# Optimization experiments

Hardware: AMD Instinct MI355X
Metric: run time of the kernel (lower is better)

Reference implementation:

```python
import jax, jax.numpy as jnp
import numpy as np

B, K, D, H = 16384, 3, 1024, 16
DH = D // H  # head_dim = 64


def setup_inputs() -> dict:
    key = jax.random.key(0)
    ks = jax.random.split(key, 12)
    s = 1.0 / np.sqrt(D)
    inp = {
        "tokens": jax.random.normal(ks[0], (B, K, D), dtype=jnp.float32),
        "ctx": jax.random.normal(ks[1], (B, 1, D), dtype=jnp.float32),
        "Wq": jax.random.uniform(ks[2], (D, D), jnp.float32, -s, s),
        "bq": jnp.zeros((D,), jnp.float32),
        "Wk": jax.random.uniform(ks[3], (D, D), jnp.float32, -s, s),
        "bk": jnp.zeros((D,), jnp.float32),
        "Wv": jax.random.uniform(ks[4], (D, D), jnp.float32, -s, s),
        "bv": jnp.zeros((D,), jnp.float32),
        "Wc": jax.random.uniform(ks[5], (D, D), jnp.float32, -s, s),
        "bc": jnp.zeros((D,), jnp.float32),
        "Wo": jax.random.uniform(ks[6], (D, D), jnp.float32, -s, s),
        "bo": jnp.zeros((D,), jnp.float32),
    }
    return inp


def _split_heads(x):
    # (B, L, D) -> (B, H, L, DH)
    Bq, L, _ = x.shape
    return x.reshape(Bq, L, H, DH).transpose(0, 2, 1, 3)


def reference(tokens, ctx, Wq, bq, Wk, bk, Wv, bv, Wc, bc, Wo, bo):
    q = _split_heads(tokens @ Wq.T + bq)          # (B,H,K,DH)
    k = _split_heads(tokens @ Wk.T + bk)          # (B,H,K,DH)
    v = _split_heads(tokens @ Wv.T + bv)          # (B,H,K,DH)
    c = _split_heads(ctx @ Wc.T + bc)             # (B,H,1,DH)
    k_ctx = k * c                                  # context-modulated keys
    v_ctx = v * c                                  # context-modulated values
    scores = jnp.einsum("bhqd,bhkd->bhqk", q, k_ctx) / jnp.sqrt(jnp.float32(DH))
    probs = jax.nn.softmax(scores, axis=-1)       # dropout p=0.0 -> identity
    out = jnp.einsum("bhqk,bhkd->bhqd", probs, v_ctx)
    out = out.transpose(0, 2, 1, 3).reshape(tokens.shape[0], K, D)  # merge heads
    return out @ Wo.T + bo
```

## Files before the change

### kernel.cpp

```cpp
#include <hip/hip_runtime.h>
#include <hip/hip_bf16.h>

#define BB 16384
#define KK 3
#define DD 1024
#define HH 16

typedef __attribute__((ext_vector_type(8))) short bf16x8;
typedef __attribute__((ext_vector_type(4))) float f32x4;
typedef unsigned int u32;

__device__ __forceinline__ void load_lds16(const void* g, void* l) {
  __builtin_amdgcn_global_load_lds(
      (const __attribute__((address_space(1))) u32*)g,
      (__attribute__((address_space(3))) u32*)l,
      16, 0, 0);
}

__device__ __forceinline__ unsigned short f2bf(float f) {
  __hip_bfloat16 h = __float2bfloat16(f);
  unsigned short u;
  __builtin_memcpy(&u, &h, 2);
  return u;
}

__device__ __forceinline__ float bf2f(unsigned short u) {
  union { float f; u32 i; } cv;
  cv.i = ((u32)u) << 16;
  return cv.f;
}

__global__ void cast_f32_bf16(const float* __restrict__ in,
                              unsigned short* __restrict__ out, int n4) {
  int stride = gridDim.x * blockDim.x;
  for (int i = blockIdx.x * blockDim.x + threadIdx.x; i < n4; i += stride) {
    float4 v = ((const float4*)in)[i];
    ushort4 o;
    o.x = f2bf(v.x);
    o.y = f2bf(v.y);
    o.z = f2bf(v.z);
    o.w = f2bf(v.w);
    ((ushort4*)out)[i] = o;
  }
}

template <bool OUT_F32>
__global__ __launch_bounds__(512, 2)
void gemm256(const __hip_bfloat16* __restrict__ A,
             const __hip_bfloat16* __restrict__ Bt,
             const float* __restrict__ bias,
             void* __restrict__ Cout,
             int M, int N, int K) {
  __shared__ __align__(128) char lds[131072];

  const int nTn = N >> 8;
  const int nwg = (M >> 8) * nTn;
  int bid = blockIdx.x;
  bid = (bid & 7) * (nwg >> 3) + (bid >> 3);
  const int tm = bid / nTn;
  const int tn = bid % nTn;

  const int tid = threadIdx.x;
  const int l = tid & 63;
  const int w = tid >> 6;
  const int wm = w >> 2;
  const int wn = w & 3;
  const int l15 = l & 15;
  const int g = l >> 4;
  const int l7 = l15 & 7;

  const int cs0 = ((g ^ l7) << 4);
  const int cs1 = (((4 | g) ^ l7) << 4);
  const int aRowB = ((wm << 7) + l15) << 7;
  const int bColB = 32768 + (((wn << 6) + l15) << 7);

  const size_t strideK = (size_t)K * 2;
  const char* Ab = (const char*)A + (size_t)tm * 256 * strideK;
  const char* Bb = (const char*)Bt + (size_t)tn * 256 * strideK;
  const size_t sOff = (size_t)(tid >> 3) * strideK +
                      (size_t)(((tid & 7) ^ ((tid >> 3) & 7)) << 4);
  const int sldst = tid << 4;

  char* const sl0 = lds;
  char* const sl1 = lds + 65536;

  f32x4 acc[8][4] = {};
  bf16x8 aF[16], bF[8];
  const int njt = K >> 7;

#define STG_A(T, H)                                                        \
  {                                                                        \
    char* d = lds + (((T) & 1) << 16) + ((H) << 14) + sldst;               \
    const char* s = Ab + ((size_t)(T) << 7) +                              \
                    ((size_t)((H) << 7)) * strideK + sOff;                 \
    load_lds16(s, d);                                                      \
    load_lds16(s + 64 * strideK, d + 8192);                                \
  }
#define STG_B(T, H)                                                        \
  {                                                                        \
    char* d = lds + (((T) & 1) << 16) + 32768 + ((H) << 14) + sldst;       \
    const char* s = Bb + ((size_t)(T) << 7) +                              \
                    ((size_t)((H) << 7)) * strideK + sOff;                 \
    load_lds16(s, d);                                                      \
    load_lds16(s + 64 * strideK, d + 8192);                                \
  }
#define RD_A2(SB, m)                                                       \
  aF[2 * (m)] = *(const bf16x8*)((SB) + aRowB + ((m) << 11) + cs0);        \
  aF[2 * (m) + 1] = *(const bf16x8*)((SB) + aRowB + ((m) << 11) + cs1);
#define RD_B2(SB, n)                                                       \
  bF[2 * (n)] = *(const bf16x8*)((SB) + bColB + ((n) << 11) + cs0);        \
  bF[2 * (n) + 1] = *(const bf16x8*)((SB) + bColB + ((n) << 11) + cs1);
#define MFMA_Q(MH, NH)                                                     \
  __builtin_amdgcn_s_setprio(1);                                           \
  _Pragma("unroll") for (int mm = 0; mm < 4; ++mm)                         \
      _Pragma("unroll") for (int nn = 0; nn < 2; ++nn)                     \
          _Pragma("unroll") for (int kh = 0; kh < 2; ++kh)                 \
              acc[(MH)*4 + mm][(NH)*2 + nn] =                              \
                  __builtin_amdgcn_mfma_f32_16x16x32_bf16(                 \
                      aF[2 * ((MH)*4 + mm) + kh],                          \
                      bF[2 * ((NH)*2 + nn) + kh],                          \
                      acc[(MH)*4 + mm][(NH)*2 + nn], 0, 0, 0);             \
  __builtin_amdgcn_s_setprio(0);
#define BAR  __builtin_amdgcn_s_barrier(); asm volatile("" ::: "memory");
#define LGKM0 asm volatile("s_waitcnt lgkmcnt(0)" ::: "memory");

  STG_A(0, 0); STG_A(0, 1); STG_B(0, 0); STG_B(0, 1);
  STG_A(1, 0); STG_A(1, 1);
  asm volatile("s_waitcnt vmcnt(4)" ::: "memory");
  BAR

  for (int j = 0; j < njt; ++j) {
    const int t1 = 2 * j + 1, t2 = 2 * j + 2, t3 = 2 * j + 3;
    const bool full = (j < njt - 1);

    RD_B2(sl0, 0) RD_B2(sl0, 1)
    RD_A2(sl0, 0) RD_A2(sl0, 1) RD_A2(sl0, 2) RD_A2(sl0, 3)
    STG_B(t1, 0)
    BAR LGKM0 MFMA_Q(0, 0) BAR
    RD_A2(sl0, 4) RD_A2(sl0, 5) RD_A2(sl0, 6) RD_A2(sl0, 7)
    STG_B(t1, 1)
    BAR LGKM0 MFMA_Q(1, 0) BAR
    RD_B2(sl0, 2) RD_B2(sl0, 3)
    if (full) STG_A(t2, 0)
    BAR LGKM0 MFMA_Q(0, 1) BAR
    if (full) STG_A(t2, 1)
    if (full) { asm volatile("s_waitcnt vmcnt(4)" ::: "memory"); }
    else      { asm volatile("s_waitcnt vmcnt(0)" ::: "memory"); }
    BAR MFMA_Q(1, 1) BAR

    RD_B2(sl1, 0) RD_B2(sl1, 1)
    RD_A2(sl1, 0) RD_A2(sl1, 1) RD_A2(sl1, 2) RD_A2(sl1, 3)
    if (full) STG_B(t2, 0)
    BAR LGKM0 MFMA_Q(0, 0) BAR
    RD_A2(sl1, 4) RD_A2(sl1, 5) RD_A2(sl1, 6) RD_A2(sl1, 7)
    if (full) STG_B(t2, 1)
    BAR LGKM0 MFMA_Q(1, 0) BAR
    RD_B2(sl1, 2) RD_B2(sl1, 3)
    if (full) STG_A(t3, 0)
    BAR LGKM0 MFMA_Q(0, 1) BAR
    if (full) STG_A(t3, 1)
    if (full) { asm volatile("s_waitcnt vmcnt(4)" ::: "memory"); }
    else      { asm volatile("s_waitcnt vmcnt(0)" ::: "memory"); }
    BAR MFMA_Q(1, 1) BAR
  }
#undef STG_A
#undef STG_B
#undef RD_A2
#undef RD_B2
#undef MFMA_Q
#undef BAR
#undef LGKM0

  const int cbase = tn * 256 + (wn << 6) + l15;
  float b4[4];
#pragma unroll
  for (int n = 0; n < 4; ++n) b4[n] = bias[cbase + (n << 4)];
  const size_t rbase = (size_t)tm * 256 + (wm << 7) + ((l >> 4) << 2);
#pragma unroll
  for (int m = 0; m < 8; ++m) {
#pragma unroll
    for (int j = 0; j < 4; ++j) {
      const size_t row = rbase + (m << 4) + j;
#pragma unroll
      for (int n = 0; n < 4; ++n) {
        const int col = cbase + (n << 4);
        float v = acc[m][n][j] + b4[n];
        if (OUT_F32)
          ((float*)Cout)[row * N + col] = v;
        else
          ((unsigned short*)Cout)[row * N + col] = f2bf(v);
      }
    }
  }
}

__global__ __launch_bounds__(256)
void attn_kernel(const unsigned short* __restrict__ QKV,
                 const unsigned short* __restrict__ Cp,
                 unsigned short* __restrict__ Out) {
  const int t = threadIdx.x;
  const int grp = (blockIdx.x << 4) + (t >> 4);
  const int x = t & 15;
  const int b = grp >> 4;
  const int h = grp & 15;

  const size_t col = (size_t)h * 64 + (x << 2);
  const size_t qbase = (size_t)b * 3 * 3072 + col;

  ushort4 cu = *(const ushort4*)&Cp[(size_t)b * 1024 + col];
  float c[4] = {bf2f(cu.x), bf2f(cu.y), bf2f(cu.z), bf2f(cu.w)};

  float q[3][4], kc[3][4], vc[3][4];
#pragma unroll
  for (int i = 0; i < 3; ++i) {
    ushort4 qu = *(const ushort4*)&QKV[qbase + (size_t)i * 3072];
    ushort4 ku = *(const ushort4*)&QKV[qbase + (size_t)i * 3072 + 1024];
    ushort4 vu = *(const ushort4*)&QKV[qbase + (size_t)i * 3072 + 2048];
    q[i][0] = bf2f(qu.x); q[i][1] = bf2f(qu.y); q[i][2] = bf2f(qu.z); q[i][3] = bf2f(qu.w);
    kc[i][0] = bf2f(ku.x) * c[0]; kc[i][1] = bf2f(ku.y) * c[1];
    kc[i][2] = bf2f(ku.z) * c[2]; kc[i][3] = bf2f(ku.w) * c[3];
    vc[i][0] = bf2f(vu.x) * c[0]; vc[i][1] = bf2f(vu.y) * c[1];
    vc[i][2] = bf2f(vu.z) * c[2]; vc[i][3] = bf2f(vu.w) * c[3];
  }

  float s[9];
#pragma unroll
  for (int i = 0; i < 3; ++i)
#pragma unroll
    for (int j = 0; j < 3; ++j)
      s[i * 3 + j] = q[i][0] * kc[j][0] + q[i][1] * kc[j][1] +
                     q[i][2] * kc[j][2] + q[i][3] * kc[j][3];

#pragma unroll
  for (int off = 8; off > 0; off >>= 1)
#pragma unroll
    for (int e = 0; e < 9; ++e)
      s[e] += __shfl_xor(s[e], off, 64);

  const float scale = 0.125f;
#pragma unroll
  for (int i = 0; i < 3; ++i) {
    float s0 = s[i * 3 + 0] * scale;
    float s1 = s[i * 3 + 1] * scale;
    float s2 = s[i * 3 + 2] * scale;
    float m = fmaxf(fmaxf(s0, s1), s2);
    float p0 = expf(s0 - m), p1 = expf(s1 - m), p2 = expf(s2 - m);
    float inv = 1.0f / (p0 + p1 + p2);
    ushort4 o;
    o.x = f2bf((p0 * vc[0][0] + p1 * vc[1][0] + p2 * vc[2][0]) * inv);
    o.y = f2bf((p0 * vc[0][1] + p1 * vc[1][1] + p2 * vc[2][1]) * inv);
    o.z = f2bf((p0 * vc[0][2] + p1 * vc[1][2] + p2 * vc[2][2]) * inv);
    o.w = f2bf((p0 * vc[0][3] + p1 * vc[1][3] + p2 * vc[2][3]) * inv);
    *(ushort4*)&Out[(size_t)(b * 3 + i) * 1024 + col] = o;
  }
}

extern "C" void kernel_launch(void* const* d_in, const int* in_sizes, int n_in,
                              void* d_out, int out_size, void* d_ws, size_t ws_size,
                              hipStream_t stream) {
  const float* tokens = (const float*)d_in[0];
  const float* ctx    = (const float*)d_in[1];
  const float* Wq     = (const float*)d_in[2];
  const float* bq     = (const float*)d_in[3];
  const float* Wk     = (const float*)d_in[4];
  const float* bk     = (const float*)d_in[5];
  const float* Wv     = (const float*)d_in[6];
  const float* bv     = (const float*)d_in[7];
  const float* Wc     = (const float*)d_in[8];
  const float* bc     = (const float*)d_in[9];
  const float* Wo     = (const float*)d_in[10];
  const float* bo     = (const float*)d_in[11];

  const int M  = BB * KK;
  const int Mc = BB;
  const int D  = DD;

  char* p = (char*)d_ws;
  auto carve = [&](size_t bytes) {
    char* r = p;
    p += (bytes + 255) & ~(size_t)255;
    return r;
  };
  unsigned short* Xb   = (unsigned short*)carve((size_t)M * D * 2);
  unsigned short* Cin  = (unsigned short*)carve((size_t)Mc * D * 2);
  unsigned short* Wqkv = (unsigned short*)carve((size_t)3 * D * D * 2);
  unsigned short* Wcb  = (unsigned short*)carve((size_t)D * D * 2);
  unsigned short* Wob  = (unsigned short*)carve((size_t)D * D * 2);
  float*          bqkv = (float*)carve((size_t)3 * D * 4);
  unsigned short* QKV  = (unsigned short*)carve((size_t)M * 3 * D * 2);
  unsigned short* Cpr  = (unsigned short*)carve((size_t)Mc * D * 2);

  hipLaunchKernelGGL(cast_f32_bf16, dim3(4096), dim3(256), 0, stream, tokens, Xb, M * D / 4);
  hipLaunchKernelGGL(cast_f32_bf16, dim3(2048), dim3(256), 0, stream, ctx, Cin, Mc * D / 4);
  hipLaunchKernelGGL(cast_f32_bf16, dim3(512), dim3(256), 0, stream, Wq, Wqkv, D * D / 4);
  hipLaunchKernelGGL(cast_f32_bf16, dim3(512), dim3(256), 0, stream, Wk, Wqkv + D * D, D * D / 4);
  hipLaunchKernelGGL(cast_f32_bf16, dim3(512), dim3(256), 0, stream, Wv, Wqkv + 2 * D * D, D * D / 4);
  hipLaunchKernelGGL(cast_f32_bf16, dim3(512), dim3(256), 0, stream, Wc, Wcb, D * D / 4);
  hipLaunchKernelGGL(cast_f32_bf16, dim3(512), dim3(256), 0, stream, Wo, Wob, D * D / 4);
  hipMemcpyAsync(bqkv, bq, D * 4, hipMemcpyDeviceToDevice, stream);
  hipMemcpyAsync(bqkv + D, bk, D * 4, hipMemcpyDeviceToDevice, stream);
  hipMemcpyAsync(bqkv + 2 * D, bv, D * 4, hipMemcpyDeviceToDevice, stream);

  hipLaunchKernelGGL((gemm256<false>), dim3((M / 256) * (3 * D / 256)), dim3(512), 0, stream,
                     (const __hip_bfloat16*)Xb, (const __hip_bfloat16*)Wqkv, bqkv,
                     (void*)QKV, M, 3 * D, D);
  hipLaunchKernelGGL((gemm256<false>), dim3((Mc / 256) * (D / 256)), dim3(512), 0, stream,
                     (const __hip_bfloat16*)Cin, (const __hip_bfloat16*)Wcb, bc,
                     (void*)Cpr, Mc, D, D);
  hipLaunchKernelGGL(attn_kernel, dim3(BB * HH / 16), dim3(256), 0, stream, QKV, Cpr, Xb);
  hipLaunchKernelGGL((gemm256<true>), dim3((M / 256) * (D / 256)), dim3(512), 0, stream,
                     (const __hip_bfloat16*)Xb, (const __hip_bfloat16*)Wob, bo,
                     d_out, M, D, D);
}
```

Measured before the change: 628.1 us.

## Fuse activation fp32-to-bf16 cast into GEMM A-loading and batch weight casts

Removes the separate cast kernels for tokens and ctx. A new GEMM kernel instead reads fp32 A directly into registers, converts it to bf16 and writes it into swizzled LDS, while B still arrives through direct global-to-LDS loads. The five weight casts are merged into one launch. This saves a full write and re-read of the bf16 activation copies. In exchange, the GEMM reads twice as many A bytes and uses a simpler double-buffered pipeline that may hide latency less well than the original gemm256.

```diff
diff --git a/kernel.cpp b/kernel.cpp
--- a/kernel.cpp
+++ b/kernel.cpp
@@ -30,17 +30,153 @@
   return cv.f;
 }
 
-__global__ void cast_f32_bf16(const float* __restrict__ in,
-                              unsigned short* __restrict__ out, int n4) {
-  int stride = gridDim.x * blockDim.x;
-  for (int i = blockIdx.x * blockDim.x + threadIdx.x; i < n4; i += stride) {
-    float4 v = ((const float4*)in)[i];
+__global__ __launch_bounds__(256)
+void cast_weights5(const float* __restrict__ Wq, const float* __restrict__ Wk,
+                   const float* __restrict__ Wv, const float* __restrict__ Wc,
+                   const float* __restrict__ Wo,
+                   unsigned short* __restrict__ Wqkv,
+                   unsigned short* __restrict__ Wcb,
+                   unsigned short* __restrict__ Wob) {
+  const int mat = blockIdx.x >> 8;
+  const int inner = blockIdx.x & 255;
+  const float* src = mat == 0 ? Wq : mat == 1 ? Wk : mat == 2 ? Wv
+                   : mat == 3 ? Wc : Wo;
+  unsigned short* dst = mat <= 2 ? Wqkv + (size_t)mat * DD * DD
+                      : mat == 3 ? Wcb : Wob;
+  const int base = inner * 1024 + threadIdx.x;
+#pragma unroll
+  for (int k = 0; k < 4; ++k) {
+    const int i = base + k * 256;
+    float4 v = ((const float4*)src)[i];
     ushort4 o;
-    o.x = f2bf(v.x);
-    o.y = f2bf(v.y);
-    o.z = f2bf(v.z);
-    o.w = f2bf(v.w);
-    ((ushort4*)out)[i] = o;
+    o.x = f2bf(v.x); o.y = f2bf(v.y); o.z = f2bf(v.z); o.w = f2bf(v.w);
+    ((ushort4*)dst)[i] = o;
+  }
+}
+
+__global__ __launch_bounds__(512, 2)
+void gemm_f32a(const float* __restrict__ A,
+               const __hip_bfloat16* __restrict__ Bt,
+               const float* __restrict__ bias,
+               unsigned short* __restrict__ Cout,
+               int M, int N, int K) {
+  __shared__ __align__(128) char lds[65536];
+
+  const int nTn = N >> 8;
+  const int nwg = (M >> 8) * nTn;
+  int bid = blockIdx.x;
+  bid = (bid & 7) * (nwg >> 3) + (bid >> 3);
+  const int tm = bid / nTn;
+  const int tn = bid % nTn;
+
+  const int tid = threadIdx.x;
+  const int l = tid & 63;
+  const int w = tid >> 6;
+  const int wm = w >> 2;
+  const int wn = w & 3;
+  const int l15 = l & 15;
+  const int g = l >> 4;
+  const int l7 = l15 & 7;
+
+  const int aBase = (l15 << 7) + (((wm << 2) + g) ^ l7) * 16;
+  const int bBase = 16384 + ((((wn & 1) << 6) + l15) << 7) +
+                    ((((wn >> 1) << 2) + g) ^ l7) * 16;
+
+  const int qa = tid & 7;
+  const int r1 = ((qa >> 2) << 7) + (tid >> 3);
+  const float* As = A + ((size_t)(tm * 256 + r1)) * K + ((qa & 3) << 3);
+  const int da = ((r1 & 127) << 7) + ((qa ^ (r1 & 7)) << 4);
+
+  const size_t strideB = (size_t)K * 2;
+  const char* Bb = (const char*)Bt + (size_t)tn * 256 * strideB;
+  const int qb = (tid & 7) ^ ((tid >> 3) & 7);
+  const size_t gb0 = (size_t)((qb >> 2) * 128 + (tid >> 3)) * strideB +
+                     (size_t)((qb & 3) << 4);
+  const size_t gb1 = gb0 + (size_t)64 * strideB;
+  const int sld = tid << 4;
+
+  f32x4 acc[8][4] = {};
+  float a0[8], a1[8];
+  const int nkt = K >> 5;
+
+#define LOAD_A(T)                                                         \
+  {                                                                       \
+    const float* s = As + ((T) << 5);                                     \
+    *(float4*)&a0[0] = *(const float4*)(s);                               \
+    *(float4*)&a0[4] = *(const float4*)(s + 4);                           \
+    *(float4*)&a1[0] = *(const float4*)(s + (size_t)64 * K);              \
+    *(float4*)&a1[4] = *(const float4*)(s + (size_t)64 * K + 4);          \
+  }
+#define LOAD_B(T)                                                         \
+  {                                                                       \
+    char* sb = lds + (((T) & 1) << 15);                                   \
+    const char* gbp = Bb + ((size_t)(T) << 6);                            \
+    load_lds16(gbp + gb0, sb + 16384 + sld);                              \
+    load_lds16(gbp + gb1, sb + 24576 + sld);                              \
+  }
+#define WRITE_A(T)                                                        \
+  {                                                                       \
+    char* sb = lds + (((T) & 1) << 15);                                   \
+    bf16x8 p0, p1;                                                        \
+    _Pragma("unroll") for (int j = 0; j < 8; ++j) {                       \
+      p0[j] = (short)f2bf(a0[j]);                                         \
+      p1[j] = (short)f2bf(a1[j]);                                         \
+    }                                                                     \
+    *(bf16x8*)(sb + da) = p0;                                             \
+    *(bf16x8*)(sb + 8192 + da) = p1;                                      \
+  }
+
+  LOAD_B(0);
+  LOAD_A(0);
+
+  for (int kt = 0; kt < nkt; ++kt) {
+    asm volatile("s_waitcnt vmcnt(0)" ::: "memory");
+    WRITE_A(kt);
+    asm volatile("s_waitcnt lgkmcnt(0)" ::: "memory");
+    __builtin_amdgcn_s_barrier();
+    asm volatile("" ::: "memory");
+
+    const char* slot = lds + ((kt & 1) << 15);
+    bf16x8 bfr[4], af[8];
+#pragma unroll
+    for (int n = 0; n < 4; ++n)
+      bfr[n] = *(const bf16x8*)(slot + bBase + (n << 11));
+#pragma unroll
+    for (int m = 0; m < 8; ++m)
+      af[m] = *(const bf16x8*)(slot + aBase + (m << 11));
+
+    if (kt + 1 < nkt) {
+      LOAD_B(kt + 1);
+      LOAD_A(kt + 1);
+    }
+
+    __builtin_amdgcn_s_setprio(1);
+#pragma unroll
+    for (int m = 0; m < 8; ++m)
+#pragma unroll
+      for (int n = 0; n < 4; ++n)
+        acc[m][n] = __builtin_amdgcn_mfma_f32_16x16x32_bf16(af[m], bfr[n],
+                                                            acc[m][n], 0, 0, 0);
+    __builtin_amdgcn_s_setprio(0);
+  }
+#undef LOAD_A
+#undef LOAD_B
+#undef WRITE_A
+
+  const int cbase = tn * 256 + (wn << 6) + l15;
+  float b4[4];
+#pragma unroll
+  for (int n = 0; n < 4; ++n) b4[n] = bias[cbase + (n << 4)];
+  const size_t rbase = (size_t)tm * 256 + (wm << 7) + ((l >> 4) << 2);
+#pragma unroll
+  for (int m = 0; m < 8; ++m) {
+#pragma unroll
+    for (int j = 0; j < 4; ++j) {
+      const size_t row = rbase + (m << 4) + j;
+#pragma unroll
+      for (int n = 0; n < 4; ++n)
+        Cout[row * N + cbase + (n << 4)] = f2bf(acc[m][n][j] + b4[n]);
+    }
   }
 }
 
@@ -281,8 +417,7 @@
     p += (bytes + 255) & ~(size_t)255;
     return r;
   };
-  unsigned short* Xb   = (unsigned short*)carve((size_t)M * D * 2);
-  unsigned short* Cin  = (unsigned short*)carve((size_t)Mc * D * 2);
+  unsigned short* AOut = (unsigned short*)carve((size_t)M * D * 2);
   unsigned short* Wqkv = (unsigned short*)carve((size_t)3 * D * D * 2);
   unsigned short* Wcb  = (unsigned short*)carve((size_t)D * D * 2);
   unsigned short* Wob  = (unsigned short*)carve((size_t)D * D * 2);
@@ -290,25 +425,18 @@
   unsigned short* QKV  = (unsigned short*)carve((size_t)M * 3 * D * 2);
   unsigned short* Cpr  = (unsigned short*)carve((size_t)Mc * D * 2);
 
-  hipLaunchKernelGGL(cast_f32_bf16, dim3(4096), dim3(256), 0, stream, tokens, Xb, M * D / 4);
-  hipLaunchKernelGGL(cast_f32_bf16, dim3(2048), dim3(256), 0, stream, ctx, Cin, Mc * D / 4);
-  hipLaunchKernelGGL(cast_f32_bf16, dim3(512), dim3(256), 0, stream, Wq, Wqkv, D * D / 4);
-  hipLaunchKernelGGL(cast_f32_bf16, dim3(512), dim3(256), 0, stream, Wk, Wqkv + D * D, D * D / 4);
-  hipLaunchKernelGGL(cast_f32_bf16, dim3(512), dim3(256), 0, stream, Wv, Wqkv + 2 * D * D, D * D / 4);
-  hipLaunchKernelGGL(cast_f32_bf16, dim3(512), dim3(256), 0, stream, Wc, Wcb, D * D / 4);
-  hipLaunchKernelGGL(cast_f32_bf16, dim3(512), dim3(256), 0, stream, Wo, Wob, D * D / 4);
+  hipLaunchKernelGGL(cast_weights5, dim3(1280), dim3(256), 0, stream,
+                     Wq, Wk, Wv, Wc, Wo, Wqkv, Wcb, Wob);
   hipMemcpyAsync(bqkv, bq, D * 4, hipMemcpyDeviceToDevice, stream);
   hipMemcpyAsync(bqkv + D, bk, D * 4, hipMemcpyDeviceToDevice, stream);
   hipMemcpyAsync(bqkv + 2 * D, bv, D * 4, hipMemcpyDeviceToDevice, stream);
 
-  hipLaunchKernelGGL((gemm256<false>), dim3((M / 256) * (3 * D / 256)), dim3(512), 0, stream,
-                     (const __hip_bfloat16*)Xb, (const __hip_bfloat16*)Wqkv, bqkv,
-                     (void*)QKV, M, 3 * D, D);
-  hipLaunchKernelGGL((gemm256<false>), dim3((Mc / 256) * (D / 256)), dim3(512), 0, stream,
-                     (const __hip_bfloat16*)Cin, (const __hip_bfloat16*)Wcb, bc,
-                     (void*)Cpr, Mc, D, D);
-  hipLaunchKernelGGL(attn_kernel, dim3(BB * HH / 16), dim3(256), 0, stream, QKV, Cpr, Xb);
+  hipLaunchKernelGGL(gemm_f32a, dim3((M / 256) * (3 * D / 256)), dim3(512), 0, stream,
+                     tokens, (const __hip_bfloat16*)Wqkv, bqkv, QKV, M, 3 * D, D);
+  hipLaunchKernelGGL(gemm_f32a, dim3((Mc / 256) * (D / 256)), dim3(512), 0, stream,
+                     ctx, (const __hip_bfloat16*)Wcb, bc, Cpr, Mc, D, D);
+  hipLaunchKernelGGL(attn_kernel, dim3(BB * HH / 16), dim3(256), 0, stream, QKV, Cpr, AOut);
   hipLaunchKernelGGL((gemm256<true>), dim3((M / 256) * (D / 256)), dim3(512), 0, stream,
-                     (const __hip_bfloat16*)Xb, (const __hip_bfloat16*)Wob, bo,
+                     (const __hip_bfloat16*)AOut, (const __hip_bfloat16*)Wob, bo,
                      d_out, M, D, D);
 }
```

Result: slower. 748.6 us (+19.2%).
